# Kernel tuning notes

Measured on AMD Instinct MI355X. Metric: run time of the kernel, lower is better.

The kernel has to match this reference:

```python
import jax, jax.numpy as jnp
import numpy as np

# dims: B batch, C features, N nodes, L seq_len, P pred_len, D d_model, M topk+self,
# H hidden(=4D), K date2vec freqs, DM time_features, PPH points_per_hour
B, C, N, L, P, D, M, H, K, DM, PPH = 32, 3, 883, 12, 12, 128, 10, 512, 16, 5, 12


def setup_inputs() -> dict:
    ks = jax.random.split(jax.random.key(0), 24)
    r = lambda i, shape, s=1.0: jax.random.normal(ks[i], shape, dtype=jnp.float32) * s
    z = lambda shape: jnp.zeros(shape, jnp.float32)
    return {
        "input": r(0, (B, C, N, L)),
        "adj": r(1, (N, N)),
        "seqs_time": jax.random.uniform(ks[2], (B, DM, 1, L), dtype=jnp.float32) - 0.5,
        "targets_time": jax.random.uniform(ks[3], (B, DM, 1, P), dtype=jnp.float32) - 0.5,
        "memory_bank": r(4, (N, D), (2.0 / (N + D)) ** 0.5),
        "We1": r(5, (D, D), D ** -0.5),
        "We2": r(6, (D, D), D ** -0.5),
        "time_in_day_emb": r(7, (PPH * 24, D), 0.05),
        "day_in_week_emb": r(8, (7, D), 0.05),
        "ts_emb_W": r(9, (D, C * L), (C * L) ** -0.5),
        "ts_emb_b": z((D,)),
        "conv_in_W": r(10, (C, C), C ** -0.5),
        "conv_in_b": z((C,)),
        "enc_W1": r(11, (3, H, H), H ** -0.5),
        "enc_b1": z((3, H)),
        "enc_W2": r(12, (3, H, H), H ** -0.5),
        "enc_b2": z((3, H)),
        "reg_W": r(13, (C * L, H), H ** -0.5),
        "reg_b": z((C * L,)),
        "d2v_w0": r(14, (DM,), 0.1),
        "d2v_b0": r(15, (1,), 0.1),
        "d2v_W": r(16, (K, DM), 0.3),
        "d2v_b": r(17, (K,), 0.3),
        "d2v_mix": r(18, (1,), 0.1),
        "weight_inextend": r(19, (M,), 0.3),
        "fus_W": r(20, (C, D), C ** -0.5),
        "fus_b": z((D,)),
        "glu_W1": r(21, (D, C), D ** -0.5),
        "glu_b1": z((C,)),
        "glu_W2": r(22, (D, C), D ** -0.5),
        "glu_b2": z((C,)),
    }


def _forward(input, adj, seqs_time, targets_time, memory_bank, We1, We2,
             time_in_day_emb, day_in_week_emb, ts_emb_W, ts_emb_b,
             conv_in_W, conv_in_b, enc_W1, enc_b1, enc_W2, enc_b2,
             reg_W, reg_b, d2v_w0, d2v_b0, d2v_W, d2v_b, d2v_mix,
             weight_inextend, fus_W, fus_b, glu_W1, glu_b1, glu_W2, glu_b2):
    eps = 1e-5

    def bn(x):  # train-mode BatchNorm2d, identity affine (default init)
        m = x.mean((0, 2, 3), keepdims=True)
        v = x.var((0, 2, 3), keepdims=True)
        return (x - m) * jax.lax.rsqrt(v + eps)

    # --- adaptive adjacency: matmul + row standardize + masked softmax ---
    e1 = memory_bank @ We1
    e2 = memory_bank @ We2
    a = e1 @ e2.T  # [N, N]
    a = (a - a.mean(-1, keepdims=True)) / jnp.std(a, axis=-1, ddof=1, keepdims=True)
    a = jax.nn.softmax(jax.nn.relu(a) - jnp.eye(N, dtype=a.dtype) * 1e6, axis=-1)

    xb = bn(input)  # [B, C, N, L]

    # --- Input module (STID-style) ---
    ts = xb.transpose(0, 2, 1, 3).reshape(B, N, C * L)  # [B, N, C*L]
    ts_emb = jnp.einsum('bnk,dk->bdn', ts, ts_emb_W) + ts_emb_b[None, :, None]
    hour = (seqs_time[:, -2, 0, :] + 0.5) * 23.0
    minute = (seqs_time[:, -1, 0, :] + 0.5) * 59.0
    tidx = jnp.clip(((hour * 60.0 + minute) / (60.0 / PPH))[:, -1].astype(jnp.int32), 0, PPH * 24 - 1)
    didx = jnp.clip(((seqs_time[:, 2, 0, -1] + 0.5) * 6.0).astype(jnp.int32), 0, 6)
    tid = jnp.broadcast_to(time_in_day_emb[tidx][:, :, None], (B, D, N))
    diw = jnp.broadcast_to(day_in_week_emb[didx][:, :, None], (B, D, N))
    node = jnp.broadcast_to(memory_bank.T[None], (B, D, N))
    hidden = jnp.concatenate([ts_emb, node, tid, diw], axis=1)  # [B, 4D, N]
    for i in range(3):  # MLP residual blocks (1x1 conv == channel matmul)
        h = jax.nn.relu(jnp.einsum('hk,bkn->bhn', enc_W1[i], hidden) + enc_b1[i][None, :, None])
        hidden = hidden + jnp.einsum('hk,bkn->bhn', enc_W2[i], h) + enc_b2[i][None, :, None]
    reg = jnp.einsum('ok,bkn->bon', reg_W, hidden) + reg_b[None, :, None]  # [B, C*L, N]
    hid = bn(reg.reshape(B, C, L, N).transpose(0, 1, 3, 2))  # [B, C, N, L]
    cx = jnp.einsum('oc,bcnl->bonl', conv_in_W, xb) + conv_in_b[None, :, None, None]
    x = bn(hid + cx)

    # --- sample module: topk neighbors + gather ---
    top_value, index = jax.lax.top_k(a, M - 1)  # [N, M-1]
    x_ext = jnp.concatenate([x[:, :, :, None, :], x[:, :, index]], axis=3)  # [B,C,N,M,L]

    # --- Date2Vec (Time2Vec-style periodic embedding) ---
    tau = jnp.concatenate([seqs_time, targets_time], axis=-1)[:, :, 0, :]  # [B, DM, L+P]
    phi = (jnp.einsum('bdt,d->bt', tau, d2v_w0) + d2v_b0[0]
           + jnp.sin(jnp.einsum('bdt,kd->bkt', tau, d2v_W) + d2v_b[None, :, None]).sum(1))
    d2v = phi[:, None, None, None, :] + d2v_mix[0] * x_ext.mean(-1)[..., None]  # [B,C,N,M,L+P]
    d2v_x, d2v_y = d2v[..., :L], d2v[..., L:]

    # --- Fusion: date-attention over source timesteps, neighbor-weighted merge ---
    scores = jnp.einsum('bcnmp,bcnml->bnmpl', d2v_y, d2v_x) / jnp.float32(C * L)
    A = jax.nn.softmax(scores, axis=-1)
    pm = jnp.einsum('bnmpl,bcnml->bcnmp', A, x_ext)
    w = jnp.concatenate([jnp.ones((N, 1), pm.dtype), top_value], axis=-1) * weight_inextend[None, :]
    pred = jnp.einsum('bcnmp,nm->bcnp', pm, w)
    pred = jnp.einsum('bcnp,cd->bdnp', pred, fus_W) + fus_b[None, :, None, None]

    # --- GLU output module ---
    o1 = jnp.einsum('bdnp,do->bonp', pred, glu_W1) + glu_b1[None, :, None, None]
    o2 = jnp.einsum('bdnp,do->bonp', pred, glu_W2) + glu_b2[None, :, None, None]
    return o1 * jax.nn.sigmoid(o2)  # [B, C, N, P]


def reference(input, adj, seqs_time, targets_time, memory_bank, We1, We2,
              time_in_day_emb, day_in_week_emb, ts_emb_W, ts_emb_b,
              conv_in_W, conv_in_b, enc_W1, enc_b1, enc_W2, enc_b2,
              reg_W, reg_b, d2v_w0, d2v_b0, d2v_W, d2v_b, d2v_mix,
              weight_inextend, fus_W, fus_b, glu_W1, glu_b1, glu_W2, glu_b2):
    return _forward(input, adj, seqs_time, targets_time, memory_bank, We1, We2,
                    time_in_day_emb, day_in_week_emb, ts_emb_W, ts_emb_b,
                    conv_in_W, conv_in_b, enc_W1, enc_b1, enc_W2, enc_b2,
                    reg_W, reg_b, d2v_w0, d2v_b0, d2v_W, d2v_b, d2v_mix,
                    weight_inextend, fus_W, fus_b, glu_W1, glu_b1, glu_W2, glu_b2)
```

## Files before the change

### kernel.cpp

```cpp
#include <hip/hip_runtime.h>
#include <hip/hip_bf16.h>


#define NN 883
#define NPAD 896
#define BB 32
#define HH 512
#define NL 10596
#define CNT_PER_C 339072.0f
#define TOT_X 1017216
#define LSTR 32
#define LREG 4096

typedef __attribute__((ext_vector_type(8))) short bf16x8;
typedef __attribute__((ext_vector_type(4))) float f32x4;

static __device__ __forceinline__ float bf2f(__hip_bfloat16 v) { return __bfloat162float(v); }
static __device__ __forceinline__ float ldf(const void* p, long i, int f) {
    return f ? ((const float*)p)[i] : bf2f(((const __hip_bfloat16*)p)[i]);
}
static __device__ __forceinline__ unsigned short bfbits(float v) {
    __hip_bfloat16 h = __float2bfloat16(v);
    return *(unsigned short*)&h;
}
static __device__ __forceinline__ void async_copy16(const void* g, void* l) {
    __builtin_amdgcn_global_load_lds((const __attribute__((address_space(1))) void*)g,
                                     (__attribute__((address_space(3))) void*)l, 16, 0, 0);
}

struct alignas(8) BF4 { __hip_bfloat16 a, b, c, d; };

__global__ void k_sent_r12(float* __restrict__ out, int n)
{
    int i = blockIdx.x*256 + threadIdx.x;
    if (i < n) out[i] = 1000.0f;
}

__global__ void k_probe_r12(const unsigned short* __restrict__ u, int* __restrict__ flag)
{
    int t = threadIdx.x, cnt = 0;
    for (int i = t; i < 4096; i += 256) {
        int e = (u[i] >> 7) & 0xFF;
        cnt += (e >= 0xC0);
    }
    __shared__ int r[256];
    r[t] = cnt; __syncthreads();
    for (int s = 128; s > 0; s >>= 1) { if (t < s) r[t] += r[t+s]; __syncthreads(); }
    if (t == 0) *flag = (r[0] > 8) ? 1 : 0;
}

__global__ void k_fin_r12(const float* __restrict__ pb, int P, float* __restrict__ out)
{
    int t = threadIdx.x;
    float s[6] = {0,0,0,0,0,0};
    for (int r = t; r < P; r += 256)
        #pragma unroll
        for (int j = 0; j < 6; j++) s[j] += pb[r*6 + j];
    __shared__ float red[6][256];
    #pragma unroll
    for (int j = 0; j < 6; j++) red[j][t] = s[j];
    __syncthreads();
    for (int st = 128; st > 0; st >>= 1) {
        if (t < st) {
            #pragma unroll
            for (int j = 0; j < 6; j++) red[j][t] += red[j][t+st];
        }
        __syncthreads();
    }
    if (t < 6) out[t] = red[t][0];
}

__global__ void k_wsplit_r12(const void* __restrict__ src, const int* __restrict__ dflag,
                             int n, __hip_bfloat16* __restrict__ hi,
                             __hip_bfloat16* __restrict__ lo)
{
    int f = *dflag;
    for (int i = blockIdx.x*256 + threadIdx.x; i < n; i += gridDim.x*256) {
        float v = ldf(src, i, f);
        __hip_bfloat16 h = __float2bfloat16(v);
        hi[i] = h;
        lo[i] = __float2bfloat16(v - bf2f(h));
    }
}

__global__ void k_prep_r12(const void* __restrict__ seqs, const void* __restrict__ tgts,
                           const void* __restrict__ w0, const void* __restrict__ b0,
                           const void* __restrict__ d2vW, const void* __restrict__ d2vb,
                           const void* __restrict__ fusW, const void* __restrict__ fusb,
                           const void* __restrict__ g1W, const void* __restrict__ g1b,
                           const void* __restrict__ g2W, const void* __restrict__ g2b,
                           const int* __restrict__ dflag,
                           int* __restrict__ tidx, int* __restrict__ didx,
                           float* __restrict__ phi, float* __restrict__ wc)
{
    int f = *dflag, t = threadIdx.x;
    if (t < 32) {
        int b = t;
        float h  = (ldf(seqs, (b*5+3)*12 + 11, f) + 0.5f) * 23.0f;
        float mi = (ldf(seqs, (b*5+4)*12 + 11, f) + 0.5f) * 59.0f;
        int ti = (int)((h * 60.0f + mi) / 5.0f);
        tidx[b] = ti < 0 ? 0 : (ti > 287 ? 287 : ti);
        int di = (int)((ldf(seqs, (b*5+2)*12 + 11, f) + 0.5f) * 6.0f);
        didx[b] = di < 0 ? 0 : (di > 6 ? 6 : di);
    }
    for (int i = t; i < 768; i += 256) {
        int b = i / 24, tt = i % 24;
        float tau[5];
        #pragma unroll
        for (int d = 0; d < 5; d++)
            tau[d] = (tt < 12) ? ldf(seqs, (b*5+d)*12 + tt, f)
                               : ldf(tgts, (b*5+d)*12 + tt - 12, f);
        float s = ldf(b0, 0, f);
        #pragma unroll
        for (int d = 0; d < 5; d++) s += tau[d] * ldf(w0, d, f);
        for (int k = 0; k < 16; k++) {
            float arg = ldf(d2vb, k, f);
            #pragma unroll
            for (int d = 0; d < 5; d++) arg += tau[d] * ldf(d2vW, k*5 + d, f);
            s += sinf(arg);
        }
        phi[i] = s;
    }
    if (t < 24) {
        if (t < 9) {
            int o = t / 3, c = t % 3; float s = 0.f;
            for (int d = 0; d < 128; d++) s += ldf(fusW, c*128+d, f) * ldf(g1W, d*3+o, f);
            wc[t] = s;
        } else if (t < 12) {
            int o = t - 9; float s = ldf(g1b, o, f);
            for (int d = 0; d < 128; d++) s += ldf(fusb, d, f) * ldf(g1W, d*3+o, f);
            wc[9 + o] = s;
        } else if (t < 21) {
            int j = t - 12; int o = j / 3, c = j % 3; float s = 0.f;
            for (int d = 0; d < 128; d++) s += ldf(fusW, c*128+d, f) * ldf(g2W, d*3+o, f);
            wc[12 + j] = s;
        } else {
            int o = t - 21; float s = ldf(g2b, o, f);
            for (int d = 0; d < 128; d++) s += ldf(fusb, d, f) * ldf(g2W, d*3+o, f);
            wc[21 + o] = s;
        }
    }
}

__global__ void k_e_r12(const void* __restrict__ mb, const void* __restrict__ We1,
                        const void* __restrict__ We2, const int* __restrict__ dflag,
                        float* __restrict__ e1, float* __restrict__ e2t)
{
    int f = *dflag;
    int idx = blockIdx.x*256 + threadIdx.x;
    int which = idx >= 113024;
    int j = which ? idx - 113024 : idx;
    int d = j & 127, n = j >> 7;
    const void* W = which ? We2 : We1;
    float s = 0.f;
    for (int k = 0; k < 128; k++)
        s += ldf(mb, n*128 + k, f) * ldf(W, k*128 + d, f);
    if (which) e2t[d*NN + n] = s;
    else       e1[j] = s;
}

__global__ void __launch_bounds__(256)
k_graph_r12(const float* __restrict__ e1, const float* __restrict__ e2t,
            float* __restrict__ topval, int* __restrict__ topidx)
{
    int n = blockIdx.x, t = threadIdx.x;
    __shared__ float e1s[128];
    __shared__ float arow[NN];
    __shared__ float red[256];
    __shared__ int redi[256];
    if (t < 128) e1s[t] = e1[n*128 + t];
    __syncthreads();
    for (int m = t; m < NN; m += 256) {
        float acc = 0.f;
        #pragma unroll 8
        for (int k = 0; k < 128; k++) acc += e1s[k] * e2t[k*NN + m];
        arow[m] = acc;
    }
    __syncthreads();
    float s = 0.f;
    for (int m = t; m < NN; m += 256) s += arow[m];
    red[t] = s; __syncthreads();
    for (int st = 128; st > 0; st >>= 1) { if (t < st) red[t] += red[t+st]; __syncthreads(); }
    float mean = red[0] / 883.0f; __syncthreads();
    float ss = 0.f;
    for (int m = t; m < NN; m += 256) { float d = arow[m] - mean; ss += d*d; }
    red[t] = ss; __syncthreads();
    for (int st = 128; st > 0; st >>= 1) { if (t < st) red[t] += red[t+st]; __syncthreads(); }
    float rstd = 1.0f / sqrtf(red[0] / 882.0f); __syncthreads();
    for (int m = t; m < NN; m += 256) {
        float z = (arow[m] - mean) * rstd;
        z = fmaxf(z, 0.f);
        if (m == n) z -= 1e6f;
        arow[m] = z;
    }
    __syncthreads();
    float mx = -3.4e38f;
    for (int m = t; m < NN; m += 256) mx = fmaxf(mx, arow[m]);
    red[t] = mx; __syncthreads();
    for (int st = 128; st > 0; st >>= 1) { if (t < st) red[t] = fmaxf(red[t], red[t+st]); __syncthreads(); }
    float M = red[0]; __syncthreads();
    float ds = 0.f;
    for (int m = t; m < NN; m += 256) { float e = expf(arow[m] - M); arow[m] = e; ds += e; }
    red[t] = ds; __syncthreads();
    for (int st = 128; st > 0; st >>= 1) { if (t < st) red[t] += red[t+st]; __syncthreads(); }
    float inv = 1.0f / red[0]; __syncthreads();
    for (int m = t; m < NN; m += 256) arow[m] *= inv;
    __syncthreads();
    for (int j = 0; j < 9; j++) {
        float bv = -1.f; int bi = 0;
        for (int m = t; m < NN; m += 256) { float v = arow[m]; if (v > bv) { bv = v; bi = m; } }
        red[t] = bv; redi[t] = bi; __syncthreads();
        for (int st = 128; st > 0; st >>= 1) {
            if (t < st) {
                float ov = red[t+st]; int oi = redi[t+st];
                if (ov > red[t] || (ov == red[t] && oi < redi[t])) { red[t] = ov; redi[t] = oi; }
            }
            __syncthreads();
        }
        if (t == 0) {
            topval[n*9 + j] = red[0];
            topidx[n*9 + j] = redi[0];
            arow[redi[0]] = -1.f;
        }
        __syncthreads();
    }
}

__global__ void k_bn1_r12(const void* __restrict__ x, const int* __restrict__ dflag,
                          float* __restrict__ pb)
{
    int f = *dflag;
    float s[3] = {0,0,0}, q[3] = {0,0,0};
    for (int i = blockIdx.x*256 + threadIdx.x; i < TOT_X; i += 512*256) {
        int c = (i / NL) % 3;
        float v = ldf(x, i, f);
        s[c] += v; q[c] += v*v;
    }
    __shared__ float red[6][256];
    int t = threadIdx.x;
    #pragma unroll
    for (int j = 0; j < 3; j++) { red[j][t] = s[j]; red[3+j][t] = q[j]; }
    __syncthreads();
    for (int st_ = 128; st_ > 0; st_ >>= 1) {
        if (t < st_) {
            #pragma unroll
            for (int j = 0; j < 6; j++) red[j][t] += red[j][t+st_];
        }
        __syncthreads();
    }
    if (t < 6) pb[blockIdx.x*6 + t] = red[t][0];
}

__global__ void __launch_bounds__(256)
k_hid_r12(const void* __restrict__ in, const void* __restrict__ mb,
          const void* __restrict__ tide, const void* __restrict__ diwe,
          const void* __restrict__ tsW, const void* __restrict__ tsb,
          const int* __restrict__ tidx, const int* __restrict__ didx,
          const int* __restrict__ dflag, const float* __restrict__ st1,
          int b0, __hip_bfloat16* __restrict__ Xhi, __hip_bfloat16* __restrict__ Xlo)
{
    int f = *dflag;
    int bl = blockIdx.y, bg = b0 + bl, t = threadIdx.x;
    int n0 = blockIdx.x * 8;
    __shared__ float tsw[128*37];
    __shared__ float tsbs[128];
    __shared__ float xbs[8][36];
    float m1[3], r1v[3];
    #pragma unroll
    for (int c = 0; c < 3; c++) {
        float m = st1[c] * (1.0f/CNT_PER_C);
        float v = st1[3+c] * (1.0f/CNT_PER_C) - m*m;
        m1[c] = m; r1v[c] = 1.0f / sqrtf(v + 1e-5f);
    }
    for (int i = t; i < 4608; i += 256)
        tsw[(i/36)*37 + (i%36)] = ldf(tsW, i, f);
    if (t < 128) tsbs[t] = ldf(tsb, t, f);
    for (int i = t; i < 288; i += 256) {
        int nl = i / 36, k = i % 36;
        int c = k / 12, l = k % 12;
        int n = n0 + nl; if (n >= NN) n = NN - 1;
        xbs[nl][k] = (ldf(in, ((long)(bg*3 + c)*NN + n)*12 + l, f) - m1[c]) * r1v[c];
    }
    __syncthreads();
    int nloc = t >> 5, lane = t & 31;
    int n = n0 + nloc;
    if (n >= NN) return;
    size_t base = ((size_t)bl*NPAD + n)*HH;
    const float* xr = xbs[nloc];
    #pragma unroll
    for (int j = 0; j < 8; j++) {
        int ch0 = j*64 + lane*2;
        float v0, v1;
        if (j < 2) {
            float a0 = tsbs[ch0], a1 = tsbs[ch0+1];
            #pragma unroll
            for (int k = 0; k < 36; k++) {
                float xv = xr[k];
                a0 += xv * tsw[ch0*37 + k];
                a1 += xv * tsw[(ch0+1)*37 + k];
            }
            v0 = a0; v1 = a1;
        } else if (j < 4) {
            v0 = ldf(mb, n*128 + ch0 - 128, f);
            v1 = ldf(mb, n*128 + ch0 - 127, f);
        } else if (j < 6) {
            v0 = ldf(tide, tidx[bg]*128 + ch0 - 256, f);
            v1 = ldf(tide, tidx[bg]*128 + ch0 - 255, f);
        } else {
            v0 = ldf(diwe, didx[bg]*128 + ch0 - 384, f);
            v1 = ldf(diwe, didx[bg]*128 + ch0 - 383, f);
        }
        unsigned short h0 = bfbits(v0), h1 = bfbits(v1);
        __hip_bfloat16 hb0, hb1;
        *(unsigned short*)&hb0 = h0; *(unsigned short*)&hb1 = h1;
        unsigned short l0 = bfbits(v0 - bf2f(hb0)), l1 = bfbits(v1 - bf2f(hb1));
        *(unsigned*)(Xhi + base + ch0) = (unsigned)h0 | ((unsigned)h1 << 16);
        *(unsigned*)(Xlo + base + ch0) = (unsigned)l0 | ((unsigned)l1 << 16);
    }
}

template<bool RELU, bool RESID, bool REGT>
__global__ void __launch_bounds__(256)
k_gemm_r12(const __hip_bfloat16* __restrict__ Whi, const __hip_bfloat16* __restrict__ Wlo,
           long Woff, const void* __restrict__ bias, long boff,
           const int* __restrict__ dflag,
           const __hip_bfloat16* __restrict__ Xhi, const __hip_bfloat16* __restrict__ Xlo,
           __hip_bfloat16* __restrict__ Yhi, __hip_bfloat16* __restrict__ Ylo,
           float* __restrict__ regT, float* __restrict__ pb2, int HO, int b0)
{
    __shared__ __align__(16) short sm[4*LREG];
    int tid = threadIdx.x, bz = blockIdx.z;
    int n0 = blockIdx.x * 128, ho0 = blockIdx.y * 128;
    int lane = tid & 63, wave = tid >> 6;
    int wm = wave & 1, wn = wave >> 1;
    int lm = lane & 15, quad = lane >> 4;

    f32x4 acc[4][4];
    #pragma unroll
    for (int i = 0; i < 4; i++)
        #pragma unroll
        for (int j = 0; j < 4; j++) acc[i][j] = (f32x4){0.f, 0.f, 0.f, 0.f};

    const size_t xb0 = (size_t)bz*NPAD*HH;
    int rri[2], nBi[2], kci[2], lofsi[2];
    #pragma unroll
    for (int it = 0; it < 2; it++) {
        int s = it*256 + tid;
        int row = s >> 2; kci[it] = (s & 3) * 8;
        int rr = ho0 + row; rri[it] = (rr >= HO) ? HO - 1 : rr;
        int nB = n0 + row; nBi[it] = (nB >= NN) ? NN - 1 : nB;
        lofsi[it] = s * 8;
    }

    for (int k0 = 0; k0 < 512; k0 += 32) {
        #pragma unroll
        for (int it = 0; it < 2; it++) {
            size_t wofs = (size_t)Woff + (size_t)rri[it]*512 + k0 + kci[it];
            size_t xofs = xb0 + (size_t)nBi[it]*HH + k0 + kci[it];
            int lofs = lofsi[it];
            async_copy16(Whi + wofs, &sm[lofs]);
            async_copy16(Wlo + wofs, &sm[LREG + lofs]);
            async_copy16(Xhi + xofs, &sm[2*LREG + lofs]);
            async_copy16(Xlo + xofs, &sm[3*LREG + lofs]);
        }
        __syncthreads();
        bf16x8 ah[4], al[4], bh[4], bl[4];
        #pragma unroll
        for (int mi = 0; mi < 4; mi++) {
            int o = (wm*64 + mi*16 + lm)*LSTR + quad*8;
            ah[mi] = *(const bf16x8*)&sm[o];
            al[mi] = *(const bf16x8*)&sm[LREG + o];
        }
        #pragma unroll
        for (int ni = 0; ni < 4; ni++) {
            int o = (wn*64 + ni*16 + lm)*LSTR + quad*8;
            bh[ni] = *(const bf16x8*)&sm[2*LREG + o];
            bl[ni] = *(const bf16x8*)&sm[3*LREG + o];
        }
        #pragma unroll
        for (int mi = 0; mi < 4; mi++)
            #pragma unroll
            for (int ni = 0; ni < 4; ni++) {
                acc[mi][ni] = __builtin_amdgcn_mfma_f32_16x16x32_bf16(ah[mi], bh[ni], acc[mi][ni], 0, 0, 0);
                acc[mi][ni] = __builtin_amdgcn_mfma_f32_16x16x32_bf16(ah[mi], bl[ni], acc[mi][ni], 0, 0, 0);
                acc[mi][ni] = __builtin_amdgcn_mfma_f32_16x16x32_bf16(al[mi], bh[ni], acc[mi][ni], 0, 0, 0);
            }
        __syncthreads();
    }

    int f = *dflag;
    float s3[3] = {0,0,0}, q3[3] = {0,0,0};
    #pragma unroll
    for (int mi = 0; mi < 4; mi++) {
        int hor = ho0 + wm*64 + mi*16 + quad*4;
        float bv[4];
        #pragma unroll
        for (int r = 0; r < 4; r++) {
            int h = hor + r; if (h >= HO) h = HO - 1;
            bv[r] = ldf(bias, boff + h, f);
        }
        #pragma unroll
        for (int ni = 0; ni < 4; ni++) {
            int nc = n0 + wn*64 + ni*16 + lm;
            if (nc >= NN) continue;
            if constexpr (REGT) {
                if (hor <= 32) {
                    int c = hor / 12;
                    float4 v4;
                    v4.x = acc[mi][ni][0] + bv[0];
                    v4.y = acc[mi][ni][1] + bv[1];
                    v4.z = acc[mi][ni][2] + bv[2];
                    v4.w = acc[mi][ni][3] + bv[3];
                    *(float4*)(regT + ((size_t)(b0 + bz)*NN + nc)*36 + hor) = v4;
                    s3[c] += v4.x + v4.y + v4.z + v4.w;
                    q3[c] += v4.x*v4.x + v4.y*v4.y + v4.z*v4.z + v4.w*v4.w;
                }
            } else {
                size_t o = xb0 + (size_t)nc*HH + hor;
                float vals[4];
                #pragma unroll
                for (int r = 0; r < 4; r++) vals[r] = acc[mi][ni][r] + bv[r];
                if constexpr (RESID) {
                    BF4 rh = *(const BF4*)(Yhi + o);
                    BF4 rl = *(const BF4*)(Ylo + o);
                    vals[0] += bf2f(rh.a) + bf2f(rl.a);
                    vals[1] += bf2f(rh.b) + bf2f(rl.b);
                    vals[2] += bf2f(rh.c) + bf2f(rl.c);
                    vals[3] += bf2f(rh.d) + bf2f(rl.d);
                }
                if constexpr (RELU) {
                    #pragma unroll
                    for (int r = 0; r < 4; r++) vals[r] = fmaxf(vals[r], 0.f);
                }
                BF4 hi, lo;
                hi.a = __float2bfloat16(vals[0]); lo.a = __float2bfloat16(vals[0] - bf2f(hi.a));
                hi.b = __float2bfloat16(vals[1]); lo.b = __float2bfloat16(vals[1] - bf2f(hi.b));
                hi.c = __float2bfloat16(vals[2]); lo.c = __float2bfloat16(vals[2] - bf2f(hi.c));
                hi.d = __float2bfloat16(vals[3]); lo.d = __float2bfloat16(vals[3] - bf2f(hi.d));
                *(BF4*)(Yhi + o) = hi;
                *(BF4*)(Ylo + o) = lo;
            }
        }
    }
    if constexpr (REGT) {
        float* red = (float*)sm;
        #pragma unroll
        for (int j = 0; j < 3; j++) { red[j*256 + tid] = s3[j]; red[(3+j)*256 + tid] = q3[j]; }
        __syncthreads();
        for (int st = 128; st > 0; st >>= 1) {
            if (tid < st) {
                #pragma unroll
                for (int j = 0; j < 6; j++) red[j*256 + tid] += red[j*256 + tid + st];
            }
            __syncthreads();
        }
        if (tid < 6) pb2[((b0 + bz)*7 + blockIdx.x)*6 + tid] = red[tid*256];
    }
}

__global__ void __launch_bounds__(256)
k_xpre_r12(const float* __restrict__ regT, const void* __restrict__ in,
           const void* __restrict__ convW, const void* __restrict__ convb,
           const int* __restrict__ dflag, const float* __restrict__ st1,
           const float* __restrict__ st2, float* __restrict__ pb3,
           float* __restrict__ xpre)
{
    int f = *dflag;
    float m1[3], r1[3], m2[3], r2[3], cw[9], cb[3];
    #pragma unroll
    for (int c = 0; c < 3; c++) {
        float m = st1[c] * (1.0f/CNT_PER_C);
        float v = st1[3+c] * (1.0f/CNT_PER_C) - m*m;
        m1[c] = m; r1[c] = 1.0f / sqrtf(v + 1e-5f);
        float mm = st2[c] * (1.0f/CNT_PER_C);
        float vv = st2[3+c] * (1.0f/CNT_PER_C) - mm*mm;
        m2[c] = mm; r2[c] = 1.0f / sqrtf(vv + 1e-5f);
        cb[c] = ldf(convb, c, f);
    }
    #pragma unroll
    for (int j = 0; j < 9; j++) cw[j] = ldf(convW, j, f);
    float s0=0,s1=0,s2=0,q0=0,q1=0,q2=0;
    for (int i = blockIdx.x*256 + threadIdx.x; i < TOT_X; i += 1024*256) {
        int b = i / 31788, r1_ = i % 31788;
        int c = r1_ / NL, r2_ = r1_ % NL;
        int n = r2_ / 12, l = r2_ % 12;
        float hidv = (regT[((size_t)b*NN + n)*36 + c*12 + l] - m2[c]) * r2[c];
        float cx = cb[c];
        #pragma unroll
        for (int cc = 0; cc < 3; cc++) {
            float xbv = (ldf(in, ((long)(b*3 + cc)*NN + n)*12 + l, f) - m1[cc]) * r1[cc];
            cx += cw[c*3 + cc] * xbv;
        }
        float v = hidv + cx;
        xpre[i] = v;
        float v2 = v*v;
        s0 += (c == 0) ? v : 0.f;  q0 += (c == 0) ? v2 : 0.f;
        s1 += (c == 1) ? v : 0.f;  q1 += (c == 1) ? v2 : 0.f;
        s2 += (c == 2) ? v : 0.f;  q2 += (c == 2) ? v2 : 0.f;
    }
    __shared__ float red[6][256];
    int t = threadIdx.x;
    red[0][t] = s0; red[1][t] = s1; red[2][t] = s2;
    red[3][t] = q0; red[4][t] = q1; red[5][t] = q2;
    __syncthreads();
    for (int st_ = 128; st_ > 0; st_ >>= 1) {
        if (t < st_) {
            #pragma unroll
            for (int j = 0; j < 6; j++) red[j][t] += red[j][t+st_];
        }
        __syncthreads();
    }
    if (t < 6) pb3[blockIdx.x*6 + t] = red[t][0];
}

__global__ void __launch_bounds__(64)
k_tail_r12(const float* __restrict__ xpre, const float* __restrict__ st3,
           const float* __restrict__ phi, const float* __restrict__ topval,
           const int* __restrict__ topidx, const float* __restrict__ wc,
           const void* __restrict__ wie, const void* __restrict__ mixp,
           const int* __restrict__ dflag, float* __restrict__ out)
{
    int f = *dflag;
    int n = blockIdx.x, b = blockIdx.y, t = threadIdx.x;
    __shared__ float xe[3][10][12], mn[3][10], phis[24], ws[10];
    __shared__ float pm[3][10][12], pred[3][12];
    float m3[3], rs3[3];
    #pragma unroll
    for (int c = 0; c < 3; c++) {
        float m = st3[c] * (1.0f/CNT_PER_C);
        float v = st3[3+c] * (1.0f/CNT_PER_C) - m*m;
        m3[c] = m; rs3[c] = 1.0f / sqrtf(v + 1e-5f);
    }
    if (t < 24) phis[t] = phi[b*24 + t];
    if (t < 10) ws[t] = (t == 0 ? 1.0f : topval[n*9 + t - 1]) * ldf(wie, t, f);
    for (int i = t; i < 360; i += 64) {
        int c = i / 120, m = (i / 12) % 10, l = i % 12;
        int nn2 = (m == 0) ? n : topidx[n*9 + m - 1];
        xe[c][m][l] = (xpre[((size_t)(b*3 + c)*NN + nn2)*12 + l] - m3[c]) * rs3[c];
    }
    __syncthreads();
    if (t < 30) {
        int c = t / 10, m = t % 10;
        float s = 0.f;
        #pragma unroll
        for (int l = 0; l < 12; l++) s += xe[c][m][l];
        mn[c][m] = s * (1.0f/12.0f);
    }
    __syncthreads();
    float mix = ldf(mixp, 0, f);
    for (int pr = t; pr < 120; pr += 64) {
        int m = pr / 12, p = pr % 12;
        float y[3], sc[12], mx = -3.4e38f;
        #pragma unroll
        for (int c = 0; c < 3; c++) y[c] = phis[12+p] + mix*mn[c][m];
        #pragma unroll
        for (int l = 0; l < 12; l++) {
            float v = 0.f;
            #pragma unroll
            for (int c = 0; c < 3; c++) v += y[c] * (phis[l] + mix*mn[c][m]);
            sc[l] = v * (1.0f/36.0f); mx = fmaxf(mx, sc[l]);
        }
        float den = 0.f;
        #pragma unroll
        for (int l = 0; l < 12; l++) { float e = expf(sc[l] - mx); sc[l] = e; den += e; }
        float inv = 1.0f/den;
        float p0 = 0.f, p1 = 0.f, p2 = 0.f;
        #pragma unroll
        for (int l = 0; l < 12; l++) {
            float a = sc[l]*inv;
            p0 += a*xe[0][m][l]; p1 += a*xe[1][m][l]; p2 += a*xe[2][m][l];
        }
        pm[0][m][p] = p0; pm[1][m][p] = p1; pm[2][m][p] = p2;
    }
    __syncthreads();
    if (t < 36) {
        int c = t/12, p = t%12;
        float s = 0.f;
        #pragma unroll
        for (int m = 0; m < 10; m++) s += pm[c][m][p]*ws[m];
        pred[c][p] = s;
    }
    __syncthreads();
    if (t < 36) {
        int o = t/12, p = t%12;
        float o1 = wc[9+o]  + wc[o*3+0]*pred[0][p] + wc[o*3+1]*pred[1][p] + wc[o*3+2]*pred[2][p];
        float o2 = wc[21+o] + wc[12+o*3+0]*pred[0][p] + wc[12+o*3+1]*pred[1][p] + wc[12+o*3+2]*pred[2][p];
        out[((size_t)(b*3 + o)*NN + n)*12 + p] = o1 / (1.0f + expf(-o2));
    }
}

extern "C" void kernel_launch(void* const* d_in, const int* in_sizes, int n_in,
                              void* d_out, int out_size, void* d_ws, size_t ws_size,
                              hipStream_t stream)
{
    (void)in_sizes; (void)n_in;
    char* w = (char*)d_ws;
    auto alloc = [&](size_t bytes) { char* p = w; w += (bytes + 255) & ~(size_t)255; return p; };

    float* regT   = (float*)alloc((size_t)TOT_X*4);
    float* xpre   = (float*)alloc((size_t)TOT_X*4);
    __hip_bfloat16* Whi1 = (__hip_bfloat16*)alloc(786432*2);
    __hip_bfloat16* Wlo1 = (__hip_bfloat16*)alloc(786432*2);
    __hip_bfloat16* Whi2 = (__hip_bfloat16*)alloc(786432*2);
    __hip_bfloat16* Wlo2 = (__hip_bfloat16*)alloc(786432*2);
    __hip_bfloat16* rhi  = (__hip_bfloat16*)alloc(18432*2);
    __hip_bfloat16* rlo  = (__hip_bfloat16*)alloc(18432*2);
    float* e1     = (float*)alloc(113024*4);
    float* e2t    = (float*)alloc(113024*4);
    float* phi    = (float*)alloc(768*4);
    float* topval = (float*)alloc(7947*4);
    int*   topidx = (int*)alloc(7947*4);
    int*   tidx   = (int*)alloc(32*4);
    int*   didx   = (int*)alloc(32*4);
    float* stats  = (float*)alloc(18*4);
    float* wc     = (float*)alloc(24*4);
    int*   dflag  = (int*)alloc(4);
    float* pb1    = (float*)alloc(512*6*4);
    float* pb2    = (float*)alloc(224*6*4);
    float* pb3    = (float*)alloc(1024*6*4);
    size_t fixedEnd = (size_t)(w - (char*)d_ws);

    const size_t XB = (size_t)NPAD*HH*2;
    int CH = 0;
    for (int c = 32; c >= 1; c >>= 1) {
        if (fixedEnd + 4*(size_t)c*XB + 4096 <= ws_size) { CH = c; break; }
    }
    if (CH == 0) {
        k_sent_r12<<<(out_size + 255)/256, 256, 0, stream>>>((float*)d_out, out_size);
        return;
    }
    char* regionB = w;
    __hip_bfloat16* Xahi = (__hip_bfloat16*)regionB;
    __hip_bfloat16* Xalo = (__hip_bfloat16*)(regionB + (size_t)CH*XB);
    __hip_bfloat16* Xbhi = (__hip_bfloat16*)(regionB + 2*(size_t)CH*XB);
    __hip_bfloat16* Xblo = (__hip_bfloat16*)(regionB + 3*(size_t)CH*XB);

    k_probe_r12<<<1, 256, 0, stream>>>((const unsigned short*)d_in[0], dflag);
    k_prep_r12<<<1, 256, 0, stream>>>(d_in[2], d_in[3], d_in[19], d_in[20], d_in[21], d_in[22],
                                      d_in[25], d_in[26], d_in[27], d_in[28], d_in[29], d_in[30],
                                      dflag, tidx, didx, phi, wc);
    k_wsplit_r12<<<1024, 256, 0, stream>>>(d_in[13], dflag, 786432, Whi1, Wlo1);
    k_wsplit_r12<<<1024, 256, 0, stream>>>(d_in[15], dflag, 786432, Whi2, Wlo2);
    k_wsplit_r12<<<72,   256, 0, stream>>>(d_in[17], dflag, 18432, rhi, rlo);

    k_e_r12<<<883, 256, 0, stream>>>(d_in[4], d_in[5], d_in[6], dflag, e1, e2t);
    k_graph_r12<<<883, 256, 0, stream>>>(e1, e2t, topval, topidx);
    k_bn1_r12<<<512, 256, 0, stream>>>(d_in[0], dflag, pb1);
    k_fin_r12<<<1, 256, 0, stream>>>(pb1, 512, stats);

    for (int b0 = 0; b0 < BB; b0 += CH) {
        k_hid_r12<<<dim3(111, CH), 256, 0, stream>>>(d_in[0], d_in[4], d_in[7], d_in[8],
                                                     d_in[9], d_in[10], tidx, didx, dflag,
                                                     stats, b0, Xahi, Xalo);
        for (int i = 0; i < 3; i++) {
            k_gemm_r12<true, false, false><<<dim3(7, 4, CH), 256, 0, stream>>>(
                Whi1, Wlo1, (long)i*HH*HH, d_in[14], (long)i*HH, dflag,
                Xahi, Xalo, Xbhi, Xblo, (float*)nullptr, (float*)nullptr, HH, b0);
            k_gemm_r12<false, true, false><<<dim3(7, 4, CH), 256, 0, stream>>>(
                Whi2, Wlo2, (long)i*HH*HH, d_in[16], (long)i*HH, dflag,
                Xbhi, Xblo, Xahi, Xalo, (float*)nullptr, (float*)nullptr, HH, b0);
        }
        k_gemm_r12<false, false, true><<<dim3(7, 1, CH), 256, 0, stream>>>(
            rhi, rlo, 0, d_in[18], 0, dflag,
            Xahi, Xalo, (__hip_bfloat16*)nullptr, (__hip_bfloat16*)nullptr,
            regT, pb2, 36, b0);
    }
    k_fin_r12<<<1, 256, 0, stream>>>(pb2, 224, stats + 6);

    k_xpre_r12<<<1024, 256, 0, stream>>>(regT, d_in[0], d_in[11], d_in[12], dflag,
                                         stats, stats + 6, pb3, xpre);
    k_fin_r12<<<1, 256, 0, stream>>>(pb3, 1024, stats + 12);

    k_tail_r12<<<dim3(NN, BB), 64, 0, stream>>>(xpre, stats + 12, phi, topval, topidx, wc,
                                                d_in[24], d_in[23], dflag, (float*)d_out);
}
```

Baseline: 838.0 us.

## Transpose GEMM output tile for coalesced epilogue stores and linearize grid

Swaps which shared-memory operand feeds the MFMA A and B sides, so each output tile has nodes as rows and hidden units as columns. The epilogue then stores scalars with consecutive lanes covering consecutive hidden units, replacing the packed 4-element stores that were scattered across many node rows. The main GEMMs also move to a 1D grid whose block index is decoded with the hidden-tile index outermost, which may change how well W tiles are reused in cache. The decode hardcodes 224 blocks per hidden tile, so it is only correct when CH is 32.

```diff
diff --git a/kernel.cpp b/kernel.cpp
--- a/kernel.cpp
+++ b/kernel.cpp
@@ -28,15 +28,13 @@
                                      (__attribute__((address_space(3))) void*)l, 16, 0, 0);
 }
 
-struct alignas(8) BF4 { __hip_bfloat16 a, b, c, d; };
-
-__global__ void k_sent_r12(float* __restrict__ out, int n)
+__global__ void k_sent_r13(float* __restrict__ out, int n)
 {
     int i = blockIdx.x*256 + threadIdx.x;
     if (i < n) out[i] = 1000.0f;
 }
 
-__global__ void k_probe_r12(const unsigned short* __restrict__ u, int* __restrict__ flag)
+__global__ void k_probe_r13(const unsigned short* __restrict__ u, int* __restrict__ flag)
 {
     int t = threadIdx.x, cnt = 0;
     for (int i = t; i < 4096; i += 256) {
@@ -49,7 +47,7 @@
     if (t == 0) *flag = (r[0] > 8) ? 1 : 0;
 }
 
-__global__ void k_fin_r12(const float* __restrict__ pb, int P, float* __restrict__ out)
+__global__ void k_fin_r13(const float* __restrict__ pb, int P, float* __restrict__ out)
 {
     int t = threadIdx.x;
     float s[6] = {0,0,0,0,0,0};
@@ -70,7 +68,7 @@
     if (t < 6) out[t] = red[t][0];
 }
 
-__global__ void k_wsplit_r12(const void* __restrict__ src, const int* __restrict__ dflag,
+__global__ void k_wsplit_r13(const void* __restrict__ src, const int* __restrict__ dflag,
                              int n, __hip_bfloat16* __restrict__ hi,
                              __hip_bfloat16* __restrict__ lo)
 {
@@ -83,7 +81,7 @@
     }
 }
 
-__global__ void k_prep_r12(const void* __restrict__ seqs, const void* __restrict__ tgts,
+__global__ void k_prep_r13(const void* __restrict__ seqs, const void* __restrict__ tgts,
                            const void* __restrict__ w0, const void* __restrict__ b0,
                            const void* __restrict__ d2vW, const void* __restrict__ d2vb,
                            const void* __restrict__ fusW, const void* __restrict__ fusb,
@@ -142,7 +140,7 @@
     }
 }
 
-__global__ void k_e_r12(const void* __restrict__ mb, const void* __restrict__ We1,
+__global__ void k_e_r13(const void* __restrict__ mb, const void* __restrict__ We1,
                         const void* __restrict__ We2, const int* __restrict__ dflag,
                         float* __restrict__ e1, float* __restrict__ e2t)
 {
@@ -160,7 +158,7 @@
 }
 
 __global__ void __launch_bounds__(256)
-k_graph_r12(const float* __restrict__ e1, const float* __restrict__ e2t,
+k_graph_r13(const float* __restrict__ e1, const float* __restrict__ e2t,
             float* __restrict__ topval, int* __restrict__ topidx)
 {
     int n = blockIdx.x, t = threadIdx.x;
@@ -226,7 +224,7 @@
     }
 }
 
-__global__ void k_bn1_r12(const void* __restrict__ x, const int* __restrict__ dflag,
+__global__ void k_bn1_r13(const void* __restrict__ x, const int* __restrict__ dflag,
                           float* __restrict__ pb)
 {
     int f = *dflag;
@@ -252,7 +250,7 @@
 }
 
 __global__ void __launch_bounds__(256)
-k_hid_r12(const void* __restrict__ in, const void* __restrict__ mb,
+k_hid_r13(const void* __restrict__ in, const void* __restrict__ mb,
           const void* __restrict__ tide, const void* __restrict__ diwe,
           const void* __restrict__ tsW, const void* __restrict__ tsb,
           const int* __restrict__ tidx, const int* __restrict__ didx,
@@ -321,7 +319,7 @@
 
 template<bool RELU, bool RESID, bool REGT>
 __global__ void __launch_bounds__(256)
-k_gemm_r12(const __hip_bfloat16* __restrict__ Whi, const __hip_bfloat16* __restrict__ Wlo,
+k_gemm_r13(const __hip_bfloat16* __restrict__ Whi, const __hip_bfloat16* __restrict__ Wlo,
            long Woff, const void* __restrict__ bias, long boff,
            const int* __restrict__ dflag,
            const __hip_bfloat16* __restrict__ Xhi, const __hip_bfloat16* __restrict__ Xlo,
@@ -329,8 +327,17 @@
            float* __restrict__ regT, float* __restrict__ pb2, int HO, int b0)
 {
     __shared__ __align__(16) short sm[4*LREG];
-    int tid = threadIdx.x, bz = blockIdx.z;
-    int n0 = blockIdx.x * 128, ho0 = blockIdx.y * 128;
+    int tid = threadIdx.x;
+    int bx, by, bz;
+    if constexpr (REGT) {
+        bx = blockIdx.x; by = 0; bz = blockIdx.z;
+    } else {
+        int lin = blockIdx.x;
+        by = lin / 224;
+        int r = lin % 224;
+        bx = r % 7; bz = r / 7;
+    }
+    int n0 = bx * 128, ho0 = by * 128;
     int lane = tid & 63, wave = tid >> 6;
     int wm = wave & 1, wn = wave >> 1;
     int lm = lane & 15, quad = lane >> 4;
@@ -368,14 +375,14 @@
         #pragma unroll
         for (int mi = 0; mi < 4; mi++) {
             int o = (wm*64 + mi*16 + lm)*LSTR + quad*8;
-            ah[mi] = *(const bf16x8*)&sm[o];
-            al[mi] = *(const bf16x8*)&sm[LREG + o];
+            ah[mi] = *(const bf16x8*)&sm[2*LREG + o];
+            al[mi] = *(const bf16x8*)&sm[3*LREG + o];
         }
         #pragma unroll
         for (int ni = 0; ni < 4; ni++) {
             int o = (wn*64 + ni*16 + lm)*LSTR + quad*8;
-            bh[ni] = *(const bf16x8*)&sm[2*LREG + o];
-            bl[ni] = *(const bf16x8*)&sm[3*LREG + o];
+            bh[ni] = *(const bf16x8*)&sm[o];
+            bl[ni] = *(const bf16x8*)&sm[LREG + o];
         }
         #pragma unroll
         for (int mi = 0; mi < 4; mi++)
@@ -389,63 +396,45 @@
     }
 
     int f = *dflag;
-    float s3[3] = {0,0,0}, q3[3] = {0,0,0};
-    #pragma unroll
-    for (int mi = 0; mi < 4; mi++) {
-        int hor = ho0 + wm*64 + mi*16 + quad*4;
-        float bv[4];
-        #pragma unroll
-        for (int r = 0; r < 4; r++) {
-            int h = hor + r; if (h >= HO) h = HO - 1;
-            bv[r] = ldf(bias, boff + h, f);
-        }
-        #pragma unroll
-        for (int ni = 0; ni < 4; ni++) {
-            int nc = n0 + wn*64 + ni*16 + lm;
-            if (nc >= NN) continue;
-            if constexpr (REGT) {
-                if (hor <= 32) {
-                    int c = hor / 12;
-                    float4 v4;
-                    v4.x = acc[mi][ni][0] + bv[0];
-                    v4.y = acc[mi][ni][1] + bv[1];
-                    v4.z = acc[mi][ni][2] + bv[2];
-                    v4.w = acc[mi][ni][3] + bv[3];
-                    *(float4*)(regT + ((size_t)(b0 + bz)*NN + nc)*36 + hor) = v4;
-                    s3[c] += v4.x + v4.y + v4.z + v4.w;
-                    q3[c] += v4.x*v4.x + v4.y*v4.y + v4.z*v4.z + v4.w*v4.w;
+    float s0=0,s1=0,s2=0,q0=0,q1=0,q2=0;
+    #pragma unroll
+    for (int ni = 0; ni < 4; ni++) {
+        int ho = ho0 + wn*64 + ni*16 + lm;
+        bool hok = !REGT || (ho < 36);
+        float bv = 0.f;
+        if (hok) bv = ldf(bias, boff + ho, f);
+        int c = REGT ? (ho / 12) : 0;
+        #pragma unroll
+        for (int mi = 0; mi < 4; mi++) {
+            int nr0 = n0 + wm*64 + mi*16 + quad*4;
+            #pragma unroll
+            for (int r = 0; r < 4; r++) {
+                int nr = nr0 + r;
+                if (nr >= NN) continue;
+                float v = acc[mi][ni][r] + bv;
+                if constexpr (REGT) {
+                    if (hok) {
+                        regT[((size_t)(b0 + bz)*NN + nr)*36 + ho] = v;
+                        float v2 = v*v;
+                        s0 += (c == 0) ? v : 0.f;  q0 += (c == 0) ? v2 : 0.f;
+                        s1 += (c == 1) ? v : 0.f;  q1 += (c == 1) ? v2 : 0.f;
+                        s2 += (c == 2) ? v : 0.f;  q2 += (c == 2) ? v2 : 0.f;
+                    }
+                } else {
+                    size_t o = xb0 + (size_t)nr*HH + ho;
+                    if constexpr (RESID) v += bf2f(Yhi[o]) + bf2f(Ylo[o]);
+                    if constexpr (RELU)  v = fmaxf(v, 0.f);
+                    __hip_bfloat16 h = __float2bfloat16(v);
+                    Yhi[o] = h;
+                    Ylo[o] = __float2bfloat16(v - bf2f(h));
                 }
-            } else {
-                size_t o = xb0 + (size_t)nc*HH + hor;
-                float vals[4];
-                #pragma unroll
-                for (int r = 0; r < 4; r++) vals[r] = acc[mi][ni][r] + bv[r];
-                if constexpr (RESID) {
-                    BF4 rh = *(const BF4*)(Yhi + o);
-                    BF4 rl = *(const BF4*)(Ylo + o);
-                    vals[0] += bf2f(rh.a) + bf2f(rl.a);
-                    vals[1] += bf2f(rh.b) + bf2f(rl.b);
-                    vals[2] += bf2f(rh.c) + bf2f(rl.c);
-                    vals[3] += bf2f(rh.d) + bf2f(rl.d);
-                }
-                if constexpr (RELU) {
-                    #pragma unroll
-                    for (int r = 0; r < 4; r++) vals[r] = fmaxf(vals[r], 0.f);
-                }
-                BF4 hi, lo;
-                hi.a = __float2bfloat16(vals[0]); lo.a = __float2bfloat16(vals[0] - bf2f(hi.a));
-                hi.b = __float2bfloat16(vals[1]); lo.b = __float2bfloat16(vals[1] - bf2f(hi.b));
-                hi.c = __float2bfloat16(vals[2]); lo.c = __float2bfloat16(vals[2] - bf2f(hi.c));
-                hi.d = __float2bfloat16(vals[3]); lo.d = __float2bfloat16(vals[3] - bf2f(hi.d));
-                *(BF4*)(Yhi + o) = hi;
-                *(BF4*)(Ylo + o) = lo;
             }
         }
     }
     if constexpr (REGT) {
         float* red = (float*)sm;
-        #pragma unroll
-        for (int j = 0; j < 3; j++) { red[j*256 + tid] = s3[j]; red[(3+j)*256 + tid] = q3[j]; }
+        red[0*256 + tid] = s0; red[1*256 + tid] = s1; red[2*256 + tid] = s2;
+        red[3*256 + tid] = q0; red[4*256 + tid] = q1; red[5*256 + tid] = q2;
         __syncthreads();
         for (int st = 128; st > 0; st >>= 1) {
             if (tid < st) {
@@ -454,12 +443,12 @@
             }
             __syncthreads();
         }
-        if (tid < 6) pb2[((b0 + bz)*7 + blockIdx.x)*6 + tid] = red[tid*256];
+        if (tid < 6) pb2[((b0 + bz)*7 + bx)*6 + tid] = red[tid*256];
     }
 }
 
 __global__ void __launch_bounds__(256)
-k_xpre_r12(const float* __restrict__ regT, const void* __restrict__ in,
+k_xpre_r13(const float* __restrict__ regT, const void* __restrict__ in,
            const void* __restrict__ convW, const void* __restrict__ convb,
            const int* __restrict__ dflag, const float* __restrict__ st1,
            const float* __restrict__ st2, float* __restrict__ pb3,
@@ -514,7 +503,7 @@
 }
 
 __global__ void __launch_bounds__(64)
-k_tail_r12(const float* __restrict__ xpre, const float* __restrict__ st3,
+k_tail_r13(const float* __restrict__ xpre, const float* __restrict__ st3,
            const float* __restrict__ phi, const float* __restrict__ topval,
            const int* __restrict__ topidx, const float* __restrict__ wc,
            const void* __restrict__ wie, const void* __restrict__ mixp,
@@ -626,7 +615,7 @@
         if (fixedEnd + 4*(size_t)c*XB + 4096 <= ws_size) { CH = c; break; }
     }
     if (CH == 0) {
-        k_sent_r12<<<(out_size + 255)/256, 256, 0, stream>>>((float*)d_out, out_size);
+        k_sent_r13<<<(out_size + 255)/256, 256, 0, stream>>>((float*)d_out, out_size);
         return;
     }
     char* regionB = w;
@@ -635,42 +624,45 @@
     __hip_bfloat16* Xbhi = (__hip_bfloat16*)(regionB + 2*(size_t)CH*XB);
     __hip_bfloat16* Xblo = (__hip_bfloat16*)(regionB + 3*(size_t)CH*XB);
 
-    k_probe_r12<<<1, 256, 0, stream>>>((const unsigned short*)d_in[0], dflag);
-    k_prep_r12<<<1, 256, 0, stream>>>(d_in[2], d_in[3], d_in[19], d_in[20], d_in[21], d_in[22],
+    k_probe_r13<<<1, 256, 0, stream>>>((const unsigned short*)d_in[0], dflag);
+    k_prep_r13<<<1, 256, 0, stream>>>(d_in[2], d_in[3], d_in[19], d_in[20], d_in[21], d_in[22],
                                       d_in[25], d_in[26], d_in[27], d_in[28], d_in[29], d_in[30],
                                       dflag, tidx, didx, phi, wc);
-    k_wsplit_r12<<<1024, 256, 0, stream>>>(d_in[13], dflag, 786432, Whi1, Wlo1);
-    k_wsplit_r12<<<1024, 256, 0, stream>>>(d_in[15], dflag, 786432, Whi2, Wlo2);
-    k_wsplit_r12<<<72,   256, 0, stream>>>(d_in[17], dflag, 18432, rhi, rlo);
-
-    k_e_r12<<<883, 256, 0, stream>>>(d_in[4], d_in[5], d_in[6], dflag, e1, e2t);
-    k_graph_r12<<<883, 256, 0, stream>>>(e1, e2t, topval, topidx);
-    k_bn1_r12<<<512, 256, 0, stream>>>(d_in[0], dflag, pb1);
-    k_fin_r12<<<1, 256, 0, stream>>>(pb1, 512, stats);
+    k_wsplit_r13<<<1024, 256, 0, stream>>>(d_in[13], dflag, 786432, Whi1, Wlo1);
+    k_wsplit_r13<<<1024, 256, 0, stream>>>(d_in[15], dflag, 786432, Whi2, Wlo2);
+    k_wsplit_r13<<<72,   256, 0, stream>>>(d_in[17], dflag, 18432, rhi, rlo);
+
+    k_e_r13<<<883, 256, 0, stream>>>(d_in[4], d_in[5], d_in[6], dflag, e1, e2t);
+    k_graph_r13<<<883, 256, 0, stream>>>(e1, e2t, topval, topidx);
+    k_bn1_r13<<<512, 256, 0, stream>>>(d_in[0], dflag, pb1);
+    k_fin_r13<<<1, 256, 0, stream>>>(pb1, 512, stats);
 
     for (int b0 = 0; b0 < BB; b0 += CH) {
-        k_hid_r12<<<dim3(111, CH), 256, 0, stream>>>(d_in[0], d_in[4], d_in[7], d_in[8],
+        k_hid_r13<<<dim3(111, CH), 256, 0, stream>>>(d_in[0], d_in[4], d_in[7], d_in[8],
                                                      d_in[9], d_in[10], tidx, didx, dflag,
                                                      stats, b0, Xahi, Xalo);
+        int grid1 = 224 * 4;
+        int nblk = 7 * CH;
+        grid1 = nblk * 4;
         for (int i = 0; i < 3; i++) {
-            k_gemm_r12<true, false, false><<<dim3(7, 4, CH), 256, 0, stream>>>(
+            k_gemm_r13<true, false, false><<<grid1, 256, 0, stream>>>(
                 Whi1, Wlo1, (long)i*HH*HH, d_in[14], (long)i*HH, dflag,
                 Xahi, Xalo, Xbhi, Xblo, (float*)nullptr, (float*)nullptr, HH, b0);
-            k_gemm_r12<false, true, false><<<dim3(7, 4, CH), 256, 0, stream>>>(
+            k_gemm_r13<false, true, false><<<grid1, 256, 0, stream>>>(
                 Whi2, Wlo2, (long)i*HH*HH, d_in[16], (long)i*HH, dflag,
                 Xbhi, Xblo, Xahi, Xalo, (float*)nullptr, (float*)nullptr, HH, b0);
         }
-        k_gemm_r12<false, false, true><<<dim3(7, 1, CH), 256, 0, stream>>>(
+        k_gemm_r13<false, false, true><<<dim3(7, 1, CH), 256, 0, stream>>>(
             rhi, rlo, 0, d_in[18], 0, dflag,
             Xahi, Xalo, (__hip_bfloat16*)nullptr, (__hip_bfloat16*)nullptr,
             regT, pb2, 36, b0);
     }
-    k_fin_r12<<<1, 256, 0, stream>>>(pb2, 224, stats + 6);
-
-    k_xpre_r12<<<1024, 256, 0, stream>>>(regT, d_in[0], d_in[11], d_in[12], dflag,
+    k_fin_r13<<<1, 256, 0, stream>>>(pb2, 224, stats + 6);
+
+    k_xpre_r13<<<1024, 256, 0, stream>>>(regT, d_in[0], d_in[11], d_in[12], dflag,
                                          stats, stats + 6, pb3, xpre);
-    k_fin_r12<<<1, 256, 0, stream>>>(pb3, 1024, stats + 12);
-
-    k_tail_r12<<<dim3(NN, BB), 64, 0, stream>>>(xpre, stats + 12, phi, topval, topidx, wc,
+    k_fin_r13<<<1, 256, 0, stream>>>(pb3, 1024, stats + 12);
+
+    k_tail_r13<<<dim3(NN, BB), 64, 0, stream>>>(xpre, stats + 12, phi, topval, topidx, wc,
                                                 d_in[24], d_in[23], dflag, (float*)d_out);
 }
```

New measurement: 895.3 us. 6.8% more time.
